# Kernel optimization log

Hardware: AMD Instinct MI355X
Metric: run time of the kernel (lower is better)

Reference implementation:

```python
import jax, jax.numpy as jnp
import numpy as np

HID = 192
HEADS = 12
INNER = HID * 64  # inner_dim = dim * dim_head(=64) per the module: 12288
SCALE = 64 ** -0.5  # module scales by default dim_head=64 regardless of true per-head dim
MASK_VAL = -1e4  # finite stand-in for -finfo.max; entmax zeroes these exactly
EPS = 1e-5


def sinusoidal_emb(n, dim, offset):
    # FixedPositionalEmbedding: cat(sin, cos) over dim/2 inverse frequencies
    inv_freq = 1.0 / (10000.0 ** (np.arange(0, dim, 2, dtype=np.float32) / dim))
    t = np.arange(n, dtype=np.float32) + offset
    sinu = t[:, None] * inv_freq[None, :]  # (n, dim/2)
    return jnp.asarray(np.concatenate([np.sin(sinu), np.cos(sinu)], axis=-1))  # (n, dim)


def entmax15(x):
    # exact alpha=1.5 entmax (Peters & Martins 2019), sort-based, over last axis
    x = x / 2.0
    x = x - jnp.max(x, axis=-1, keepdims=True)
    z = -jnp.sort(-x, axis=-1)  # descending
    n = x.shape[-1]
    k = jnp.arange(1, n + 1, dtype=x.dtype)
    cs = jnp.cumsum(z, axis=-1)
    css = jnp.cumsum(z * z, axis=-1)
    mean = cs / k
    ss = css - cs * mean  # = k * running variance
    delta = (1.0 - ss) / k
    tau = mean - jnp.sqrt(jnp.maximum(delta, 0.0))
    support = jnp.sum((tau <= z).astype(jnp.int32), axis=-1, keepdims=True)
    tau_star = jnp.take_along_axis(tau, support - 1, axis=-1)
    return jnp.square(jnp.maximum(x - tau_star, 0.0))


def setup_inputs() -> dict:
    key = jax.random.key(0)
    ks = jax.random.split(key, 8)
    b, lc, lq = 16, 512, 64
    c = jax.random.normal(ks[0], (b, lc, HID), dtype=jnp.float32)
    q = jax.random.normal(ks[1], (b, lq, HID), dtype=jnp.float32)
    c_mask = jnp.ones((b, lc), dtype=bool)
    q_mask = jnp.ones((b, lq), dtype=bool)
    g = jnp.ones((1,), dtype=jnp.float32)  # ScaleNorm gain
    s_in = HID ** -0.5
    Wq = jax.random.normal(ks[2], (HID, INNER), dtype=jnp.float32) * s_in
    Wk = jax.random.normal(ks[3], (HID, INNER), dtype=jnp.float32) * s_in
    Wv = jax.random.normal(ks[4], (HID, INNER), dtype=jnp.float32) * s_in
    Wo = jax.random.normal(ks[5], (INNER, HID), dtype=jnp.float32) * (INNER ** -0.5)
    bo = jnp.zeros((HID,), dtype=jnp.float32)
    return {"c": c, "q": q, "c_mask": c_mask, "q_mask": q_mask,
            "g": g, "Wq": Wq, "Wk": Wk, "Wv": Wv, "Wo": Wo, "bo": bo}


def reference(c, q, c_mask, q_mask, g, Wq, Wk, Wv, Wo, bo):
    b, lc, _ = c.shape
    lq = q.shape[1]
    residual = c
    # pre-norm ScaleNorm applied to x (=c) only; context q is NOT normed
    nrm = jnp.maximum(jnp.linalg.norm(c, axis=-1, keepdims=True), EPS)
    xn = c / nrm * g
    # position-infused attention: offset = k_len - q_len
    q_input = xn + sinusoidal_emb(lc, HID, lq - lc)[None]
    k_input = q + sinusoidal_emb(lq, HID, 0)[None]
    v_input = q  # v uses raw kv_input (no positional emb)
    d_head = INNER // HEADS
    qh = jnp.einsum('bie,ef->bif', q_input, Wq).reshape(b, lc, HEADS, d_head).transpose(0, 2, 1, 3)
    kh = jnp.einsum('bje,ef->bjf', k_input, Wk).reshape(b, lq, HEADS, d_head).transpose(0, 2, 1, 3)
    vh = jnp.einsum('bje,ef->bjf', v_input, Wv).reshape(b, lq, HEADS, d_head).transpose(0, 2, 1, 3)
    dots = jnp.einsum('bhid,bhjd->bhij', qh, kh) * SCALE  # (b,h,lc,lq)
    input_mask = c_mask[:, None, :, None] & q_mask[:, None, None, :]
    dots = jnp.where(input_mask, dots, MASK_VAL)
    attn = entmax15(dots)
    out = jnp.einsum('bhij,bhjd->bhid', attn, vh)
    out = out.transpose(0, 2, 1, 3).reshape(b, lc, INNER)
    out = jnp.einsum('bif,fe->bie', out, Wo) + bo
    att = out + residual  # Residual
    return jnp.concatenate([c, att], axis=-1)  # (b, lc, 2*HID)
```

## Files before the change

kernel.cpp:

```cpp
#include <hip/hip_runtime.h>


typedef __attribute__((ext_vector_type(8))) short short8;
typedef __attribute__((ext_vector_type(4))) float f32x4;
typedef unsigned short u16;

#define WIDX(h, rt, kk, quad, lid) ((size_t)(((((h)*12 + (rt))*32 + (kk))*4 + (quad))*16 + (lid)) * 8)
#define QIDX(b, it, kk, quad, lid) ((size_t)(((((b)*32 + (it))*6 + (kk))*4 + (quad))*16 + (lid)) * 8)
#define RIDX(rt, kk, quad, lid)    ((size_t)((((rt)*6 + (kk))*4 + (quad))*16 + (lid)) * 8)

static __device__ __forceinline__ u16 f2bf(float f){
  union { float f; unsigned int i; } v; v.f = f;
  unsigned int x = v.i;
  return (u16)((x + 0x7FFFu + ((x >> 16) & 1u)) >> 16);
}
static __device__ __forceinline__ f32x4 mfma16(short8 a, short8 b, f32x4 c){
  return __builtin_amdgcn_mfma_f32_16x16x32_bf16(a, b, c, 0, 0, 0);
}
static __device__ __forceinline__ short8 cvt8(const float* p){
  float4 x = *(const float4*)p;
  float4 y = *(const float4*)(p + 4);
  short8 r;
  r[0] = (short)f2bf(x.x); r[1] = (short)f2bf(x.y);
  r[2] = (short)f2bf(x.z); r[3] = (short)f2bf(x.w);
  r[4] = (short)f2bf(y.x); r[5] = (short)f2bf(y.y);
  r[6] = (short)f2bf(y.z); r[7] = (short)f2bf(y.w);
  return r;
}

__global__ __launch_bounds__(256) void k_prep_all(
    const float* __restrict__ Wq, const float* __restrict__ Wk, const float* __restrict__ Wv,
    const float* __restrict__ Wo, const float* __restrict__ q, const float* __restrict__ c,
    const float* __restrict__ gp,
    u16* __restrict__ wqb, u16* __restrict__ wkb, u16* __restrict__ wvb,
    u16* __restrict__ WoT, u16* __restrict__ qb,
    u16* __restrict__ qin, u16* __restrict__ kin, float* __restrict__ out){
  __shared__ __align__(16) u16 tile[64][80];
  int bid = blockIdx.x;

  if (bid < 3552){
    size_t t = (size_t)bid * 256 + threadIdx.x;
    size_t base = t * 8;
    if (base < 7077888){
      const float* src; u16* dst; size_t off;
      if (base < 2359296){ src = Wq; dst = wqb; off = base; }
      else if (base < 4718592){ src = Wk; dst = wkb; off = base - 2359296; }
      else { src = Wv; dst = wvb; off = base - 4718592; }
      int r = (int)(off / 12288);
      int k = (int)(off - (size_t)r * 12288);
      int h = k >> 10, kr = k & 1023;
      *reinterpret_cast<short8*>(dst + WIDX(h, r >> 4, kr >> 5, (kr & 31) >> 3, r & 15))
          = cvt8(src + off);
    } else {
      size_t off = base - 7077888;
      int r = (int)(off / 192);
      int e = (int)(off - (size_t)r * 192);
      *reinterpret_cast<short8*>(qb + RIDX(r >> 4, e >> 5, (e & 31) >> 3, r & 15))
          = cvt8(q + off);
    }
    return;
  }

  if (bid < 4128){
    int tb = bid - 3552;
    int dt = tb / 3, gt = tb - (tb / 3) * 3;
    int t = threadIdx.x;
    int r0 = t >> 3, c0 = (t & 7) * 8;
    #pragma unroll
    for (int p = 0; p < 2; p++){
      int r = p * 32 + r0;
      const float* src = Wo + (size_t)(dt * 64 + r) * 192 + gt * 64 + c0;
      *reinterpret_cast<short8*>(&tile[r][c0]) = cvt8(src);
    }
    __syncthreads();
    int h  = dt >> 4;
    int kk = ((dt & 15) * 64 + c0) >> 5;
    int qd = (c0 & 31) >> 3;
    #pragma unroll
    for (int p = 0; p < 2; p++){
      int gl = p * 32 + r0;
      int g  = gt * 64 + gl;
      unsigned int wv4[4];
      #pragma unroll
      for (int qq = 0; qq < 4; qq++){
        unsigned int lo = tile[c0 + 2 * qq][gl];
        unsigned int hi = tile[c0 + 2 * qq + 1][gl];
        wv4[qq] = lo | (hi << 16);
      }
      uint4 pk; pk.x = wv4[0]; pk.y = wv4[1]; pk.z = wv4[2]; pk.w = wv4[3];
      *reinterpret_cast<uint4*>(WoT + WIDX(h, g >> 4, kk, qd, g & 15)) = pk;
    }
    return;
  }

  const float KLOG = 0.13841367062030675f;
  int w = threadIdx.x >> 6;
  int lane = threadIdx.x & 63;
  int row = (bid - 4128) * 4 + w;
  float g = gp[0];
  if (row < 8192){
    int i = row & 511;
    int b = row >> 9, it = i >> 4, lid16 = i & 15;
    const float* src = c + (size_t)row * 192;
    float x0 = src[lane], x1 = src[lane + 64], x2 = src[lane + 128];
    float* oc = out + (size_t)row * 384;
    oc[lane] = x0; oc[lane + 64] = x1; oc[lane + 128] = x2;
    float ss = x0 * x0 + x1 * x1 + x2 * x2;
    #pragma unroll
    for (int m = 1; m < 64; m <<= 1) ss += __shfl_xor(ss, m);
    float nrm = fmaxf(sqrtf(ss), 1e-5f);
    float sc = g / nrm;
    float t = (float)i - 448.0f;
    #pragma unroll
    for (int kds = 0; kds < 3; kds++){
      int e = lane + kds * 64;
      float base = (kds == 0 ? x0 : (kds == 1 ? x1 : x2)) * sc;
      int f = (e < 96) ? e : e - 96;
      float invf = exp2f(-KLOG * (float)f);
      float ang = t * invf;
      float pe = (e < 96) ? sinf(ang) : cosf(ang);
      qin[QIDX(b, it, e >> 5, (e & 31) >> 3, lid16) + (e & 7)] = f2bf(base + pe);
    }
  } else {
    int r = row - 8192;
    int j = r & 63;
    int rt = r >> 4, lid16 = r & 15;
    const float* src = q + (size_t)r * 192;
    float t = (float)j;
    #pragma unroll
    for (int kds = 0; kds < 3; kds++){
      int e = lane + kds * 64;
      int f = (e < 96) ? e : e - 96;
      float invf = exp2f(-KLOG * (float)f);
      float ang = t * invf;
      float pe = (e < 96) ? sinf(ang) : cosf(ang);
      kin[RIDX(rt, e >> 5, (e & 31) >> 3, lid16) + (e & 7)] = f2bf(src[e] + pe);
    }
  }
}

__global__ __launch_bounds__(256) void k_mnw(const u16* __restrict__ wqb, const u16* __restrict__ wkb,
                                             const u16* __restrict__ wvb, const u16* __restrict__ WoT,
                                             const u16* __restrict__ kin, const u16* __restrict__ qb,
                                             u16* __restrict__ W2t, u16* __restrict__ ut){
  __shared__ __align__(16) u16 Mst[32][200];

  int bid = blockIdx.x;
  int sh  = bid % 24;
  int et  = bid / 24;
  int sel = sh / 12, h = sh - 12 * (sh / 12);
  int w = threadIdx.x >> 6;
  int lane = threadIdx.x & 63;
  int lid = lane & 15, quad = lane >> 4;

  {
    const u16* Ab = (sel ? WoT : wqb);
    const u16* Bb = (sel ? wvb : wkb);
    const u16* A0 = Ab + WIDX(h, et * 2,     0, quad, lid);
    const u16* A1 = Ab + WIDX(h, et * 2 + 1, 0, quad, lid);
    const u16* B0 = Bb + WIDX(h, w * 3,      0, quad, lid);
    const u16* B1 = Bb + WIDX(h, w * 3 + 1,  0, quad, lid);
    const u16* B2 = Bb + WIDX(h, w * 3 + 2,  0, quad, lid);

    f32x4 acc[2][3];
    #pragma unroll
    for (int a = 0; a < 2; a++)
      #pragma unroll
      for (int ct = 0; ct < 3; ct++) acc[a][ct] = (f32x4){0.f, 0.f, 0.f, 0.f};

    for (int kk = 0; kk < 32; kk++){
      short8 a0 = *(const short8*)(A0 + kk * 512);
      short8 a1 = *(const short8*)(A1 + kk * 512);
      short8 b0 = *(const short8*)(B0 + kk * 512);
      short8 b1 = *(const short8*)(B1 + kk * 512);
      short8 b2 = *(const short8*)(B2 + kk * 512);
      acc[0][0] = mfma16(a0, b0, acc[0][0]);
      acc[0][1] = mfma16(a0, b1, acc[0][1]);
      acc[0][2] = mfma16(a0, b2, acc[0][2]);
      acc[1][0] = mfma16(a1, b0, acc[1][0]);
      acc[1][1] = mfma16(a1, b1, acc[1][1]);
      acc[1][2] = mfma16(a1, b2, acc[1][2]);
    }

    #pragma unroll
    for (int a = 0; a < 2; a++)
      #pragma unroll
      for (int ct = 0; ct < 3; ct++){
        int col = w * 48 + ct * 16 + lid;
        #pragma unroll
        for (int r = 0; r < 4; r++){
          int rl = a * 16 + quad * 4 + r;
          Mst[rl][col] = f2bf(acc[a][ct][r]);
        }
      }
  }
  __syncthreads();

  if (sel == 0){
    for (int u = w; u < 32; u += 4){
      int b = u >> 1, nt = u & 1;
      const u16* b0 = kin + RIDX(b * 4 + nt * 2,     0, quad, lid);
      const u16* b1 = kin + RIDX(b * 4 + nt * 2 + 1, 0, quad, lid);
      f32x4 acc[2][2];
      #pragma unroll
      for (int a = 0; a < 2; a++)
        #pragma unroll
        for (int bb = 0; bb < 2; bb++) acc[a][bb] = (f32x4){0.f, 0.f, 0.f, 0.f};
      #pragma unroll
      for (int kk = 0; kk < 6; kk++){
        short8 A0 = *(const short8*)&Mst[lid][quad * 8 + kk * 32];
        short8 A1 = *(const short8*)&Mst[16 + lid][quad * 8 + kk * 32];
        short8 Bf0 = *(const short8*)(b0 + kk * 512);
        short8 Bf1 = *(const short8*)(b1 + kk * 512);
        acc[0][0] = mfma16(A0, Bf0, acc[0][0]);
        acc[0][1] = mfma16(A0, Bf1, acc[0][1]);
        acc[1][0] = mfma16(A1, Bf0, acc[1][0]);
        acc[1][1] = mfma16(A1, Bf1, acc[1][1]);
      }
      u16* dst = W2t + (size_t)(b * 12 + h) * 12288;
      int qc_lo = (quad >> 1);
      int j8    = (quad & 1) * 4;
      #pragma unroll
      for (int a = 0; a < 2; a++)
        #pragma unroll
        for (int bb = 0; bb < 2; bb++){
          int jt = nt * 2 + bb;
          int qc = a * 2 + qc_lo;
          uint2 pk;
          pk.x = (unsigned)f2bf(acc[a][bb][0] * 0.0625f) | ((unsigned)f2bf(acc[a][bb][1] * 0.0625f) << 16);
          pk.y = (unsigned)f2bf(acc[a][bb][2] * 0.0625f) | ((unsigned)f2bf(acc[a][bb][3] * 0.0625f) << 16);
          *reinterpret_cast<uint2*>(dst + (size_t)((((jt * 6 + et) * 4 + qc) * 16 + lid) * 8 + j8)) = pk;
        }
    }
  } else {
    for (int u = w; u < 32; u += 4){
      int b = u >> 1, mt = u & 1;
      const u16* a0 = qb + RIDX(b * 4 + mt * 2,     0, quad, lid);
      const u16* a1 = qb + RIDX(b * 4 + mt * 2 + 1, 0, quad, lid);
      f32x4 acc[2][2];
      #pragma unroll
      for (int a = 0; a < 2; a++)
        #pragma unroll
        for (int bb = 0; bb < 2; bb++) acc[a][bb] = (f32x4){0.f, 0.f, 0.f, 0.f};
      #pragma unroll
      for (int kk = 0; kk < 6; kk++){
        short8 Af0 = *(const short8*)(a0 + kk * 512);
        short8 Af1 = *(const short8*)(a1 + kk * 512);
        short8 B0 = *(const short8*)&Mst[lid][quad * 8 + kk * 32];
        short8 B1 = *(const short8*)&Mst[16 + lid][quad * 8 + kk * 32];
        acc[0][0] = mfma16(Af0, B0, acc[0][0]);
        acc[0][1] = mfma16(Af0, B1, acc[0][1]);
        acc[1][0] = mfma16(Af1, B0, acc[1][0]);
        acc[1][1] = mfma16(Af1, B1, acc[1][1]);
      }
      u16* dst = ut + (size_t)(b * 12 + h) * 12288;
      int qc_lo = (quad >> 1);
      int j8    = (quad & 1) * 4;
      #pragma unroll
      for (int a = 0; a < 2; a++)
        #pragma unroll
        for (int bb = 0; bb < 2; bb++){
          int gt = et * 2 + bb;
          int qc = a * 2 + qc_lo;
          uint2 pk;
          pk.x = (unsigned)f2bf(acc[a][bb][0]) | ((unsigned)f2bf(acc[a][bb][1]) << 16);
          pk.y = (unsigned)f2bf(acc[a][bb][2]) | ((unsigned)f2bf(acc[a][bb][3]) << 16);
          *reinterpret_cast<uint2*>(dst + (size_t)((((gt * 2 + mt) * 4 + qc) * 16 + lid) * 8 + j8)) = pk;
        }
    }
  }
}

__global__ __launch_bounds__(256, 2) void k_attn(const u16* __restrict__ qin, const u16* __restrict__ W2t,
                                                 const u16* __restrict__ ut, const float* __restrict__ c,
                                                 const float* __restrict__ bo, float* __restrict__ out){
  __shared__ __align__(16) u16 attb[4][16][72];
  __shared__ __align__(16) float part[4][16][193];

  int bid = blockIdx.x;
  int r   = bid >> 3;
  int b   = (bid & 7) + ((r >> 5) << 3);
  int i0  = (r & 31) << 4;

  int w    = threadIdx.x >> 6;
  int lane = threadIdx.x & 63;
  int lid = lane & 15, quad = lane >> 4;

  short8 qf[6];
  {
    const u16* qbase = qin + QIDX(b, i0 >> 4, 0, quad, lid);
    #pragma unroll
    for (int kk = 0; kk < 6; kk++) qf[kk] = *(const short8*)(qbase + kk * 512);
  }

  f32x4 acc[12];
  #pragma unroll
  for (int gt = 0; gt < 12; gt++) acc[gt] = (f32x4){0.f, 0.f, 0.f, 0.f};

  const u16* W2b = W2t + (size_t)(b * 12) * 12288;
  const u16* utb = ut  + (size_t)(b * 12) * 12288;

  for (int hh = 0; hh < 3; hh++){
    int h = w * 3 + hh;
    f32x4 d[4];
    #pragma unroll
    for (int jt = 0; jt < 4; jt++) d[jt] = (f32x4){0.f, 0.f, 0.f, 0.f};
    #pragma unroll
    for (int jt = 0; jt < 4; jt++){
      const u16* wrow = W2b + (size_t)h * 12288 + (size_t)(jt * 3072) + quad * 128 + lid * 8;
      #pragma unroll
      for (int kk = 0; kk < 6; kk++){
        short8 Wf = *(const short8*)(wrow + kk * 512);
        d[jt] = mfma16(Wf, qf[kk], d[jt]);
      }
    }

    float m = d[0][0];
    #pragma unroll
    for (int jt = 0; jt < 4; jt++)
      #pragma unroll
      for (int r4 = 0; r4 < 4; r4++) m = fmaxf(m, d[jt][r4]);
    m = fmaxf(m, __shfl_xor(m, 16));
    m = fmaxf(m, __shfl_xor(m, 32));
    float tau = m - 1.0f;
    for (int it = 0; it < 12; it++){
      float s1 = 0.f, s2 = 0.f;
      #pragma unroll
      for (int jt = 0; jt < 4; jt++){
        #pragma unroll
        for (int r4 = 0; r4 < 4; r4++){
          float tv = fmaxf(d[jt][r4] - tau, 0.f);
          s1 += tv; s2 = fmaf(tv, tv, s2);
        }
      }
      s1 += __shfl_xor(s1, 16); s2 += __shfl_xor(s2, 16);
      s1 += __shfl_xor(s1, 32); s2 += __shfl_xor(s2, 32);
      s1 = fmaxf(s1, 1e-20f);
      tau += (s2 - 1.0f) * 0.5f / s1;
    }

    asm volatile("" ::: "memory");
    #pragma unroll
    for (int jt = 0; jt < 4; jt++){
      float p0 = fmaxf(d[jt][0] - tau, 0.f);
      float p1 = fmaxf(d[jt][1] - tau, 0.f);
      float p2 = fmaxf(d[jt][2] - tau, 0.f);
      float p3 = fmaxf(d[jt][3] - tau, 0.f);
      uint2 pk;
      pk.x = (unsigned)f2bf(p0 * p0) | ((unsigned)f2bf(p1 * p1) << 16);
      pk.y = (unsigned)f2bf(p2 * p2) | ((unsigned)f2bf(p3 * p3) << 16);
      *reinterpret_cast<uint2*>(&attb[w][lid][jt * 16 + quad * 4]) = pk;
    }
    asm volatile("s_waitcnt lgkmcnt(0)" ::: "memory");
    __builtin_amdgcn_sched_barrier(0);

    short8 A0 = *(const short8*)&attb[w][lid][quad * 8];
    short8 A1 = *(const short8*)&attb[w][lid][quad * 8 + 32];
    #pragma unroll
    for (int gt = 0; gt < 12; gt++){
      const u16* urow = utb + (size_t)h * 12288 + (size_t)(gt * 1024) + quad * 128 + lid * 8;
      short8 B0 = *(const short8*)(urow);
      short8 B1 = *(const short8*)(urow + 512);
      acc[gt] = mfma16(A0, B0, acc[gt]);
      acc[gt] = mfma16(A1, B1, acc[gt]);
    }
  }

  #pragma unroll
  for (int gt = 0; gt < 12; gt++){
    #pragma unroll
    for (int r4 = 0; r4 < 4; r4++)
      part[w][quad * 4 + r4][gt * 16 + lid] = acc[gt][r4];
  }
  __syncthreads();
  {
    int ti = threadIdx.x >> 4;
    int e0 = (threadIdx.x & 15) * 12;
    size_t base = (size_t)(b * 512 + i0 + ti);
    #pragma unroll
    for (int k = 0; k < 12; k++){
      int e = e0 + k;
      float s = part[0][ti][e] + part[1][ti][e] + part[2][ti][e] + part[3][ti][e];
      out[base * 384 + 192 + e] = s + bo[e] + c[base * 192 + e];
    }
  }
}

extern "C" void kernel_launch(void* const* d_in, const int* in_sizes, int n_in,
                              void* d_out, int out_size, void* d_ws, size_t ws_size,
                              hipStream_t stream) {
  (void)in_sizes; (void)n_in; (void)out_size; (void)ws_size;
  const float* c  = (const float*)d_in[0];
  const float* q  = (const float*)d_in[1];
  const float* g  = (const float*)d_in[4];
  const float* Wq = (const float*)d_in[5];
  const float* Wk = (const float*)d_in[6];
  const float* Wv = (const float*)d_in[7];
  const float* Wo = (const float*)d_in[8];
  const float* bo = (const float*)d_in[9];
  float* out = (float*)d_out;

  u16* ws  = (u16*)d_ws;
  u16* wqb = ws;
  u16* wkb = wqb + 2359296;
  u16* wvb = wkb + 2359296;
  u16* WoT = wvb + 2359296;
  u16* W2t = WoT + 2359296;
  u16* ut  = W2t + 2359296;
  u16* qb  = ut  + 2359296;
  u16* qin = qb  + 196608;
  u16* kin = qin + 1572864;

  k_prep_all<<<6432, 256, 0, stream>>>(Wq, Wk, Wv, Wo, q, c, g,
                                       wqb, wkb, wvb, WoT, qb, qin, kin, out);
  k_mnw<<<144, 256, 0, stream>>>(wqb, wkb, wvb, WoT, kin, qb, W2t, ut);
  k_attn<<<512, 256, 0, stream>>>(qin, W2t, ut, c, bo, out);
}
```

Baseline: 167.8 us.

## Split attention heads across more blocks and add a final reduction kernel

The attention kernel now gives each block 4 heads (one per wave) instead of all 12, so the grid triples to 1536 blocks with higher occupancy (launch bounds 256,4). Each block writes per-head-group partial outputs to a workspace buffer, and a new k_final kernel sums the three partials and adds bias and residual. k_mnw also halves its row tile, doubling its grid from 144 to 288 blocks. The aim is better GPU fill and fewer registers per block, paid for with an extra launch and an extra round trip of fp32 partials through global memory.

```diff
diff --git a/kernel.cpp b/kernel.cpp
--- a/kernel.cpp
+++ b/kernel.cpp
@@ -143,7 +143,7 @@
                                              const u16* __restrict__ wvb, const u16* __restrict__ WoT,
                                              const u16* __restrict__ kin, const u16* __restrict__ qb,
                                              u16* __restrict__ W2t, u16* __restrict__ ut){
-  __shared__ __align__(16) u16 Mst[32][200];
+  __shared__ __align__(16) u16 Mst[16][200];
 
   int bid = blockIdx.x;
   int sh  = bid % 24;
@@ -156,133 +156,108 @@
   {
     const u16* Ab = (sel ? WoT : wqb);
     const u16* Bb = (sel ? wvb : wkb);
-    const u16* A0 = Ab + WIDX(h, et * 2,     0, quad, lid);
-    const u16* A1 = Ab + WIDX(h, et * 2 + 1, 0, quad, lid);
-    const u16* B0 = Bb + WIDX(h, w * 3,      0, quad, lid);
-    const u16* B1 = Bb + WIDX(h, w * 3 + 1,  0, quad, lid);
-    const u16* B2 = Bb + WIDX(h, w * 3 + 2,  0, quad, lid);
-
-    f32x4 acc[2][3];
-    #pragma unroll
-    for (int a = 0; a < 2; a++)
-      #pragma unroll
-      for (int ct = 0; ct < 3; ct++) acc[a][ct] = (f32x4){0.f, 0.f, 0.f, 0.f};
+    const u16* A0 = Ab + WIDX(h, et,        0, quad, lid);
+    const u16* B0 = Bb + WIDX(h, w * 3,     0, quad, lid);
+    const u16* B1 = Bb + WIDX(h, w * 3 + 1, 0, quad, lid);
+    const u16* B2 = Bb + WIDX(h, w * 3 + 2, 0, quad, lid);
+
+    f32x4 acc[3];
+    #pragma unroll
+    for (int ct = 0; ct < 3; ct++) acc[ct] = (f32x4){0.f, 0.f, 0.f, 0.f};
 
     for (int kk = 0; kk < 32; kk++){
       short8 a0 = *(const short8*)(A0 + kk * 512);
-      short8 a1 = *(const short8*)(A1 + kk * 512);
       short8 b0 = *(const short8*)(B0 + kk * 512);
       short8 b1 = *(const short8*)(B1 + kk * 512);
       short8 b2 = *(const short8*)(B2 + kk * 512);
-      acc[0][0] = mfma16(a0, b0, acc[0][0]);
-      acc[0][1] = mfma16(a0, b1, acc[0][1]);
-      acc[0][2] = mfma16(a0, b2, acc[0][2]);
-      acc[1][0] = mfma16(a1, b0, acc[1][0]);
-      acc[1][1] = mfma16(a1, b1, acc[1][1]);
-      acc[1][2] = mfma16(a1, b2, acc[1][2]);
-    }
-
-    #pragma unroll
-    for (int a = 0; a < 2; a++)
-      #pragma unroll
-      for (int ct = 0; ct < 3; ct++){
-        int col = w * 48 + ct * 16 + lid;
-        #pragma unroll
-        for (int r = 0; r < 4; r++){
-          int rl = a * 16 + quad * 4 + r;
-          Mst[rl][col] = f2bf(acc[a][ct][r]);
-        }
-      }
+      acc[0] = mfma16(a0, b0, acc[0]);
+      acc[1] = mfma16(a0, b1, acc[1]);
+      acc[2] = mfma16(a0, b2, acc[2]);
+    }
+
+    #pragma unroll
+    for (int ct = 0; ct < 3; ct++){
+      int col = w * 48 + ct * 16 + lid;
+      #pragma unroll
+      for (int r = 0; r < 4; r++)
+        Mst[quad * 4 + r][col] = f2bf(acc[ct][r]);
+    }
   }
   __syncthreads();
+
+  int kk_e = et >> 1;
+  int qce  = (et & 1) * 2 + (quad >> 1);
+  int j8   = (quad & 1) * 4;
 
   if (sel == 0){
     for (int u = w; u < 32; u += 4){
       int b = u >> 1, nt = u & 1;
       const u16* b0 = kin + RIDX(b * 4 + nt * 2,     0, quad, lid);
       const u16* b1 = kin + RIDX(b * 4 + nt * 2 + 1, 0, quad, lid);
-      f32x4 acc[2][2];
-      #pragma unroll
-      for (int a = 0; a < 2; a++)
-        #pragma unroll
-        for (int bb = 0; bb < 2; bb++) acc[a][bb] = (f32x4){0.f, 0.f, 0.f, 0.f};
+      f32x4 acc2[2];
+      acc2[0] = (f32x4){0.f, 0.f, 0.f, 0.f};
+      acc2[1] = (f32x4){0.f, 0.f, 0.f, 0.f};
       #pragma unroll
       for (int kk = 0; kk < 6; kk++){
         short8 A0 = *(const short8*)&Mst[lid][quad * 8 + kk * 32];
-        short8 A1 = *(const short8*)&Mst[16 + lid][quad * 8 + kk * 32];
         short8 Bf0 = *(const short8*)(b0 + kk * 512);
         short8 Bf1 = *(const short8*)(b1 + kk * 512);
-        acc[0][0] = mfma16(A0, Bf0, acc[0][0]);
-        acc[0][1] = mfma16(A0, Bf1, acc[0][1]);
-        acc[1][0] = mfma16(A1, Bf0, acc[1][0]);
-        acc[1][1] = mfma16(A1, Bf1, acc[1][1]);
+        acc2[0] = mfma16(A0, Bf0, acc2[0]);
+        acc2[1] = mfma16(A0, Bf1, acc2[1]);
       }
       u16* dst = W2t + (size_t)(b * 12 + h) * 12288;
-      int qc_lo = (quad >> 1);
-      int j8    = (quad & 1) * 4;
-      #pragma unroll
-      for (int a = 0; a < 2; a++)
-        #pragma unroll
-        for (int bb = 0; bb < 2; bb++){
-          int jt = nt * 2 + bb;
-          int qc = a * 2 + qc_lo;
-          uint2 pk;
-          pk.x = (unsigned)f2bf(acc[a][bb][0] * 0.0625f) | ((unsigned)f2bf(acc[a][bb][1] * 0.0625f) << 16);
-          pk.y = (unsigned)f2bf(acc[a][bb][2] * 0.0625f) | ((unsigned)f2bf(acc[a][bb][3] * 0.0625f) << 16);
-          *reinterpret_cast<uint2*>(dst + (size_t)((((jt * 6 + et) * 4 + qc) * 16 + lid) * 8 + j8)) = pk;
-        }
+      #pragma unroll
+      for (int bb = 0; bb < 2; bb++){
+        int jt = nt * 2 + bb;
+        uint2 pk;
+        pk.x = (unsigned)f2bf(acc2[bb][0] * 0.0625f) | ((unsigned)f2bf(acc2[bb][1] * 0.0625f) << 16);
+        pk.y = (unsigned)f2bf(acc2[bb][2] * 0.0625f) | ((unsigned)f2bf(acc2[bb][3] * 0.0625f) << 16);
+        *reinterpret_cast<uint2*>(dst + (size_t)((((jt * 6 + kk_e) * 4 + qce) * 16 + lid) * 8 + j8)) = pk;
+      }
     }
   } else {
     for (int u = w; u < 32; u += 4){
       int b = u >> 1, mt = u & 1;
       const u16* a0 = qb + RIDX(b * 4 + mt * 2,     0, quad, lid);
       const u16* a1 = qb + RIDX(b * 4 + mt * 2 + 1, 0, quad, lid);
-      f32x4 acc[2][2];
-      #pragma unroll
-      for (int a = 0; a < 2; a++)
-        #pragma unroll
-        for (int bb = 0; bb < 2; bb++) acc[a][bb] = (f32x4){0.f, 0.f, 0.f, 0.f};
+      f32x4 acc2[2];
+      acc2[0] = (f32x4){0.f, 0.f, 0.f, 0.f};
+      acc2[1] = (f32x4){0.f, 0.f, 0.f, 0.f};
       #pragma unroll
       for (int kk = 0; kk < 6; kk++){
         short8 Af0 = *(const short8*)(a0 + kk * 512);
         short8 Af1 = *(const short8*)(a1 + kk * 512);
         short8 B0 = *(const short8*)&Mst[lid][quad * 8 + kk * 32];
-        short8 B1 = *(const short8*)&Mst[16 + lid][quad * 8 + kk * 32];
-        acc[0][0] = mfma16(Af0, B0, acc[0][0]);
-        acc[0][1] = mfma16(Af0, B1, acc[0][1]);
-        acc[1][0] = mfma16(Af1, B0, acc[1][0]);
-        acc[1][1] = mfma16(Af1, B1, acc[1][1]);
+        acc2[0] = mfma16(Af0, B0, acc2[0]);
+        acc2[1] = mfma16(Af1, B0, acc2[1]);
       }
       u16* dst = ut + (size_t)(b * 12 + h) * 12288;
-      int qc_lo = (quad >> 1);
-      int j8    = (quad & 1) * 4;
-      #pragma unroll
-      for (int a = 0; a < 2; a++)
-        #pragma unroll
-        for (int bb = 0; bb < 2; bb++){
-          int gt = et * 2 + bb;
-          int qc = a * 2 + qc_lo;
-          uint2 pk;
-          pk.x = (unsigned)f2bf(acc[a][bb][0]) | ((unsigned)f2bf(acc[a][bb][1]) << 16);
-          pk.y = (unsigned)f2bf(acc[a][bb][2]) | ((unsigned)f2bf(acc[a][bb][3]) << 16);
-          *reinterpret_cast<uint2*>(dst + (size_t)((((gt * 2 + mt) * 4 + qc) * 16 + lid) * 8 + j8)) = pk;
-        }
-    }
-  }
-}
-
-__global__ __launch_bounds__(256, 2) void k_attn(const u16* __restrict__ qin, const u16* __restrict__ W2t,
-                                                 const u16* __restrict__ ut, const float* __restrict__ c,
-                                                 const float* __restrict__ bo, float* __restrict__ out){
+      #pragma unroll
+      for (int a = 0; a < 2; a++){
+        int qcj = a * 2 + (quad >> 1);
+        uint2 pk;
+        pk.x = (unsigned)f2bf(acc2[a][0]) | ((unsigned)f2bf(acc2[a][1]) << 16);
+        pk.y = (unsigned)f2bf(acc2[a][2]) | ((unsigned)f2bf(acc2[a][3]) << 16);
+        *reinterpret_cast<uint2*>(dst + (size_t)((((et * 2 + mt) * 4 + qcj) * 16 + lid) * 8 + j8)) = pk;
+      }
+    }
+  }
+}
+
+__global__ __launch_bounds__(256, 4) void k_attn_p(const u16* __restrict__ qin, const u16* __restrict__ W2t,
+                                                   const u16* __restrict__ ut, float* __restrict__ pout){
   __shared__ __align__(16) u16 attb[4][16][72];
-  __shared__ __align__(16) float part[4][16][193];
-
-  int bid = blockIdx.x;
-  int r   = bid >> 3;
-  int b   = (bid & 7) + ((r >> 5) << 3);
-  int i0  = (r & 31) << 4;
+  __shared__ __align__(16) float part[4][16][97];
+
+  int bid  = blockIdx.x;
+  int slot = bid >> 3;
+  int b    = (bid & 7) + ((slot / 96) << 3);
+  int rem  = slot - (slot / 96) * 96;
+  int i0   = (rem / 3) << 4;
+  int hg   = rem - (rem / 3) * 3;
 
   int w    = threadIdx.x >> 6;
+  int h    = hg * 4 + w;
   int lane = threadIdx.x & 63;
   int lid = lane & 15, quad = lane >> 4;
 
@@ -293,97 +268,117 @@
     for (int kk = 0; kk < 6; kk++) qf[kk] = *(const short8*)(qbase + kk * 512);
   }
 
-  f32x4 acc[12];
+  const u16* W2b = W2t + ((size_t)(b * 12 + h)) * 12288;
+  const u16* utb = ut  + ((size_t)(b * 12 + h)) * 12288;
+
+  f32x4 d[4];
   #pragma unroll
-  for (int gt = 0; gt < 12; gt++) acc[gt] = (f32x4){0.f, 0.f, 0.f, 0.f};
-
-  const u16* W2b = W2t + (size_t)(b * 12) * 12288;
-  const u16* utb = ut  + (size_t)(b * 12) * 12288;
-
-  for (int hh = 0; hh < 3; hh++){
-    int h = w * 3 + hh;
-    f32x4 d[4];
-    #pragma unroll
-    for (int jt = 0; jt < 4; jt++) d[jt] = (f32x4){0.f, 0.f, 0.f, 0.f};
+  for (int jt = 0; jt < 4; jt++) d[jt] = (f32x4){0.f, 0.f, 0.f, 0.f};
+  #pragma unroll
+  for (int jt = 0; jt < 4; jt++){
+    const u16* wrow = W2b + (size_t)(jt * 3072) + quad * 128 + lid * 8;
+    #pragma unroll
+    for (int kk = 0; kk < 6; kk++){
+      short8 Wf = *(const short8*)(wrow + kk * 512);
+      d[jt] = mfma16(Wf, qf[kk], d[jt]);
+    }
+  }
+
+  float m = d[0][0];
+  #pragma unroll
+  for (int jt = 0; jt < 4; jt++)
+    #pragma unroll
+    for (int r4 = 0; r4 < 4; r4++) m = fmaxf(m, d[jt][r4]);
+  m = fmaxf(m, __shfl_xor(m, 16));
+  m = fmaxf(m, __shfl_xor(m, 32));
+  float tau = m - 1.0f;
+  for (int it = 0; it < 12; it++){
+    float s1 = 0.f, s2 = 0.f;
     #pragma unroll
     for (int jt = 0; jt < 4; jt++){
-      const u16* wrow = W2b + (size_t)h * 12288 + (size_t)(jt * 3072) + quad * 128 + lid * 8;
-      #pragma unroll
-      for (int kk = 0; kk < 6; kk++){
-        short8 Wf = *(const short8*)(wrow + kk * 512);
-        d[jt] = mfma16(Wf, qf[kk], d[jt]);
-      }
-    }
-
-    float m = d[0][0];
-    #pragma unroll
-    for (int jt = 0; jt < 4; jt++)
-      #pragma unroll
-      for (int r4 = 0; r4 < 4; r4++) m = fmaxf(m, d[jt][r4]);
-    m = fmaxf(m, __shfl_xor(m, 16));
-    m = fmaxf(m, __shfl_xor(m, 32));
-    float tau = m - 1.0f;
-    for (int it = 0; it < 12; it++){
-      float s1 = 0.f, s2 = 0.f;
-      #pragma unroll
-      for (int jt = 0; jt < 4; jt++){
-        #pragma unroll
-        for (int r4 = 0; r4 < 4; r4++){
-          float tv = fmaxf(d[jt][r4] - tau, 0.f);
-          s1 += tv; s2 = fmaf(tv, tv, s2);
-        }
-      }
-      s1 += __shfl_xor(s1, 16); s2 += __shfl_xor(s2, 16);
-      s1 += __shfl_xor(s1, 32); s2 += __shfl_xor(s2, 32);
-      s1 = fmaxf(s1, 1e-20f);
-      tau += (s2 - 1.0f) * 0.5f / s1;
-    }
-
-    asm volatile("" ::: "memory");
-    #pragma unroll
-    for (int jt = 0; jt < 4; jt++){
-      float p0 = fmaxf(d[jt][0] - tau, 0.f);
-      float p1 = fmaxf(d[jt][1] - tau, 0.f);
-      float p2 = fmaxf(d[jt][2] - tau, 0.f);
-      float p3 = fmaxf(d[jt][3] - tau, 0.f);
-      uint2 pk;
-      pk.x = (unsigned)f2bf(p0 * p0) | ((unsigned)f2bf(p1 * p1) << 16);
-      pk.y = (unsigned)f2bf(p2 * p2) | ((unsigned)f2bf(p3 * p3) << 16);
-      *reinterpret_cast<uint2*>(&attb[w][lid][jt * 16 + quad * 4]) = pk;
-    }
-    asm volatile("s_waitcnt lgkmcnt(0)" ::: "memory");
-    __builtin_amdgcn_sched_barrier(0);
-
-    short8 A0 = *(const short8*)&attb[w][lid][quad * 8];
-    short8 A1 = *(const short8*)&attb[w][lid][quad * 8 + 32];
-    #pragma unroll
-    for (int gt = 0; gt < 12; gt++){
-      const u16* urow = utb + (size_t)h * 12288 + (size_t)(gt * 1024) + quad * 128 + lid * 8;
+      #pragma unroll
+      for (int r4 = 0; r4 < 4; r4++){
+        float tv = fmaxf(d[jt][r4] - tau, 0.f);
+        s1 += tv; s2 = fmaf(tv, tv, s2);
+      }
+    }
+    s1 += __shfl_xor(s1, 16); s2 += __shfl_xor(s2, 16);
+    s1 += __shfl_xor(s1, 32); s2 += __shfl_xor(s2, 32);
+    s1 = fmaxf(s1, 1e-20f);
+    tau += (s2 - 1.0f) * 0.5f / s1;
+  }
+
+  #pragma unroll
+  for (int jt = 0; jt < 4; jt++){
+    float p0 = fmaxf(d[jt][0] - tau, 0.f);
+    float p1 = fmaxf(d[jt][1] - tau, 0.f);
+    float p2 = fmaxf(d[jt][2] - tau, 0.f);
+    float p3 = fmaxf(d[jt][3] - tau, 0.f);
+    uint2 pk;
+    pk.x = (unsigned)f2bf(p0 * p0) | ((unsigned)f2bf(p1 * p1) << 16);
+    pk.y = (unsigned)f2bf(p2 * p2) | ((unsigned)f2bf(p3 * p3) << 16);
+    *reinterpret_cast<uint2*>(&attb[w][lid][jt * 16 + quad * 4]) = pk;
+  }
+  asm volatile("s_waitcnt lgkmcnt(0)" ::: "memory");
+  __builtin_amdgcn_sched_barrier(0);
+
+  short8 A0 = *(const short8*)&attb[w][lid][quad * 8];
+  short8 A1 = *(const short8*)&attb[w][lid][quad * 8 + 32];
+
+  float* pbase = pout + (size_t)hg * 1572864 + (size_t)(b * 512 + i0) * 192;
+
+  #pragma unroll
+  for (int ch = 0; ch < 2; ch++){
+    f32x4 a6[6];
+    #pragma unroll
+    for (int g = 0; g < 6; g++){
+      int gt = ch * 6 + g;
+      const u16* urow = utb + (size_t)(gt * 1024) + quad * 128 + lid * 8;
       short8 B0 = *(const short8*)(urow);
       short8 B1 = *(const short8*)(urow + 512);
-      acc[gt] = mfma16(A0, B0, acc[gt]);
-      acc[gt] = mfma16(A1, B1, acc[gt]);
-    }
-  }
-
-  #pragma unroll
-  for (int gt = 0; gt < 12; gt++){
-    #pragma unroll
-    for (int r4 = 0; r4 < 4; r4++)
-      part[w][quad * 4 + r4][gt * 16 + lid] = acc[gt][r4];
-  }
-  __syncthreads();
-  {
-    int ti = threadIdx.x >> 4;
-    int e0 = (threadIdx.x & 15) * 12;
-    size_t base = (size_t)(b * 512 + i0 + ti);
-    #pragma unroll
-    for (int k = 0; k < 12; k++){
-      int e = e0 + k;
-      float s = part[0][ti][e] + part[1][ti][e] + part[2][ti][e] + part[3][ti][e];
-      out[base * 384 + 192 + e] = s + bo[e] + c[base * 192 + e];
-    }
-  }
+      f32x4 t = (f32x4){0.f, 0.f, 0.f, 0.f};
+      t = mfma16(A0, B0, t);
+      t = mfma16(A1, B1, t);
+      a6[g] = t;
+    }
+    #pragma unroll
+    for (int g = 0; g < 6; g++)
+      #pragma unroll
+      for (int r4 = 0; r4 < 4; r4++)
+        part[w][quad * 4 + r4][g * 16 + lid] = a6[g][r4];
+    __syncthreads();
+    {
+      int row = threadIdx.x >> 4;
+      int c0  = (threadIdx.x & 15) * 6;
+      #pragma unroll
+      for (int k = 0; k < 6; k++){
+        int col = c0 + k;
+        float s = part[0][row][col] + part[1][row][col]
+                + part[2][row][col] + part[3][row][col];
+        pbase[(size_t)row * 192 + ch * 96 + col] = s;
+      }
+    }
+    if (ch == 0) __syncthreads();
+  }
+}
+
+__global__ __launch_bounds__(256) void k_final(const float* __restrict__ pout, const float* __restrict__ c,
+                                               const float* __restrict__ bo, float* __restrict__ out){
+  int idx = blockIdx.x * 256 + threadIdx.x;
+  int row = idx / 48;
+  int e0  = (idx - row * 48) * 4;
+  size_t off = (size_t)row * 192 + e0;
+  float4 p0 = *reinterpret_cast<const float4*>(pout + off);
+  float4 p1 = *reinterpret_cast<const float4*>(pout + 1572864 + off);
+  float4 p2 = *reinterpret_cast<const float4*>(pout + 3145728 + off);
+  float4 cv = *reinterpret_cast<const float4*>(c + off);
+  float4 bv = *reinterpret_cast<const float4*>(bo + e0);
+  float4 o;
+  o.x = ((p0.x + p1.x) + p2.x) + bv.x + cv.x;
+  o.y = ((p0.y + p1.y) + p2.y) + bv.y + cv.y;
+  o.z = ((p0.z + p1.z) + p2.z) + bv.z + cv.z;
+  o.w = ((p0.w + p1.w) + p2.w) + bv.w + cv.w;
+  *reinterpret_cast<float4*>(out + (size_t)row * 384 + 192 + e0) = o;
 }
 
 extern "C" void kernel_launch(void* const* d_in, const int* in_sizes, int n_in,
@@ -410,9 +405,11 @@
   u16* qb  = ut  + 2359296;
   u16* qin = qb  + 196608;
   u16* kin = qin + 1572864;
+  float* pout = (float*)(kin + 196608);
 
   k_prep_all<<<6432, 256, 0, stream>>>(Wq, Wk, Wv, Wo, q, c, g,
                                        wqb, wkb, wvb, WoT, qb, qin, kin, out);
-  k_mnw<<<144, 256, 0, stream>>>(wqb, wkb, wvb, WoT, kin, qb, W2t, ut);
-  k_attn<<<512, 256, 0, stream>>>(qin, W2t, ut, c, bo, out);
-}
+  k_mnw<<<288, 256, 0, stream>>>(wqb, wkb, wvb, WoT, kin, qb, W2t, ut);
+  k_attn_p<<<1536, 256, 0, stream>>>(qin, W2t, ut, pout);
+  k_final<<<1536, 256, 0, stream>>>(pout, c, bo, out);
+}
```

Measured after the change: 162.4 us. 3.2% less time.
